# Optimization experiments

Measured on AMD Instinct MI355X. Metric: run time of the kernel, lower is better.

Reference implementation:

```python
import jax, jax.numpy as jnp
import numpy as np

B, TAU, M, NX, NY = 256, 128, 3, 8, 8
N = NX + NY                 # 16 total sensors
D = 2 * N * N               # d_model = 512
NHEAD = 8
DFF = 2048


def _layer_norm(x, g, b, eps=1e-5):
    mu = jnp.mean(x, axis=-1, keepdims=True)
    var = jnp.mean((x - mu) ** 2, axis=-1, keepdims=True)
    return (x - mu) / jnp.sqrt(var + eps) * g + b


def _mha(x, wi, bi, wo, bo):
    Bq, S, Dm = x.shape
    hd = Dm // NHEAD
    qkv = x @ wi.T + bi                         # (B,S,3D)
    q, k, v = jnp.split(qkv, 3, axis=-1)
    sh = lambda t: t.reshape(Bq, S, NHEAD, hd).transpose(0, 2, 1, 3)
    q, k, v = sh(q), sh(k), sh(v)
    att = jax.nn.softmax(jnp.einsum('bhqd,bhkd->bhqk', q, k) / jnp.sqrt(jnp.float32(hd)), axis=-1)
    o = jnp.einsum('bhqk,bhkd->bhqd', att, v).transpose(0, 2, 1, 3).reshape(Bq, S, Dm)
    return o @ wo.T + bo


def poly_roots(c):
    # companion-matrix roots; c[..., 0] is the leading coefficient
    n = c.shape[-1] - 1
    first = (-c[..., 1:] / c[..., :1])[..., None, :]                      # (..., 1, n)
    below = jnp.broadcast_to(jnp.eye(n - 1, n, dtype=c.dtype), c.shape[:-1] + (n - 1, n))
    return jnp.linalg.eigvals(jnp.concatenate([first, below], axis=-2))   # (..., n)


def root_music_doa(Rz, m):
    # Rz: (B, n, n) Hermitian PSD (gram + eps*I) -> eigh == eig sorted by |lambda|
    n = Rz.shape[-1]
    w, v = jnp.linalg.eigh(Rz)                  # ascending real eigenvalues
    Un = v[..., : n - m]                        # noise subspace (smallest n-m)
    F = Un @ jnp.conj(jnp.swapaxes(Un, -1, -2))
    # sum of each diagonal, offsets -(n-1)..(n-1) -> 2n-1 poly coefficients
    coeffs = jnp.stack([jnp.sum(jnp.diagonal(F, offset=o, axis1=-2, axis2=-1), axis=-1)
                        for o in range(-(n - 1), n)], axis=-1)
    roots = poly_roots(coeffs)                  # (B, 2n-2)
    # sort by closeness to unit circle; push roots with |r|>=1 to the back
    keyv = jnp.abs(jnp.abs(roots) - 1.0) + jnp.where(jnp.abs(roots) < 1.0, 0.0, 1e6)
    sel = jnp.take_along_axis(roots, jnp.argsort(keyv, axis=-1)[..., :m], axis=-1)
    # dist=0.5, f=1 -> 1/(2*pi*dist*f) = 1/pi
    return jnp.arcsin(jnp.angle(sel) / jnp.pi)  # (B, m)


def setup_inputs() -> dict:
    key = jax.random.key(0)
    ks = jax.random.split(key, 12)
    rn = lambda k, s: 0.02 * jax.random.normal(k, s, jnp.float32)
    return {
        'Rx_tau': jax.random.normal(ks[0], (B, TAU, 2 * N, N), jnp.float32),
        'in_proj_w': rn(ks[1], (3 * D, D)), 'in_proj_b': jnp.zeros((3 * D,), jnp.float32),
        'out_proj_w': rn(ks[2], (D, D)), 'out_proj_b': jnp.zeros((D,), jnp.float32),
        'ln1_g': jnp.ones((D,), jnp.float32), 'ln1_b': jnp.zeros((D,), jnp.float32),
        'ffn_w1': rn(ks[3], (DFF, D)), 'ffn_b1': jnp.zeros((DFF,), jnp.float32),
        'ffn_w2': rn(ks[4], (D, DFF)), 'ffn_b2': jnp.zeros((D,), jnp.float32),
        'ln2_g': jnp.ones((D,), jnp.float32), 'ln2_b': jnp.zeros((D,), jnp.float32),
        'fcx_w': rn(ks[5], (2 * NX * NX, D)), 'fcx_b': jnp.zeros((2 * NX * NX,), jnp.float32),
        'fcy_w': rn(ks[6], (2 * NY * NY, D)), 'fcy_b': jnp.zeros((2 * NY * NY,), jnp.float32),
        'mlp_w1': rn(ks[7], (256, 2 * M)), 'mlp_b1': jnp.zeros((256,), jnp.float32),
        'mlp_w2': rn(ks[8], (256, 256)), 'mlp_b2': jnp.zeros((256,), jnp.float32),
        'mlp_w3': rn(ks[9], (2 * M, 256)), 'mlp_b3': jnp.zeros((2 * M,), jnp.float32),
    }


def reference(Rx_tau, in_proj_w, in_proj_b, out_proj_w, out_proj_b, ln1_g, ln1_b,
              ffn_w1, ffn_b1, ffn_w2, ffn_b2, ln2_g, ln2_b,
              fcx_w, fcx_b, fcy_w, fcy_b,
              mlp_w1, mlp_b1, mlp_w2, mlp_b2, mlp_w3, mlp_b3):
    x = Rx_tau.reshape(Rx_tau.shape[0], -1, D)  # (B, tau, 512)
    # post-LN TransformerEncoderLayer (eval: dropout off)
    x = _layer_norm(x + _mha(x, in_proj_w, in_proj_b, out_proj_w, out_proj_b), ln1_g, ln1_b)
    ff = jnp.maximum(x @ ffn_w1.T + ffn_b1, 0.0) @ ffn_w2.T + ffn_b2
    x = _layer_norm(x + ff, ln2_g, ln2_b)
    x = jnp.mean(x, axis=1)                     # (B, D)
    Rx = (x @ fcx_w.T + fcx_b).reshape(-1, 2 * NX, NX)
    Ry = (x @ fcy_w.T + fcy_b).reshape(-1, 2 * NY, NY)
    Kx = jax.lax.complex(Rx[:, :NX], Rx[:, NX:])
    Ky = jax.lax.complex(Ry[:, :NY], Ry[:, NY:])
    # gram_diagonal_overload: K^H K + eps*I, eps=1
    Rz_x = jnp.einsum('bji,bjk->bik', jnp.conj(Kx), Kx) + jnp.eye(NX, dtype=Kx.dtype)
    Rz_y = jnp.einsum('bji,bjk->bik', jnp.conj(Ky), Ky) + jnp.eye(NY, dtype=Ky.dtype)
    doa_t = root_music_doa(Rz_x, M)
    doa_p = root_music_doa(Rz_y, M)
    h = jnp.concatenate([doa_t, doa_p], axis=-1).astype(jnp.float32)  # (B, 2M)
    h = jnp.maximum(h @ mlp_w1.T + mlp_b1, 0.0)
    h = jnp.maximum(h @ mlp_w2.T + mlp_b2, 0.0)
    outs = h @ mlp_w3.T + mlp_b3
    return outs[:, :M], outs[:, M:]
```

## Files before the change

kernel.cpp:

```cpp
#include <hip/hip_runtime.h>
#include <math.h>

#define S_LEN 128
#define D_MODEL 512
#define B_SZ 256
#define NHEADS 8
#define HD 64
#define DFFN 2048
#define PI_D 3.14159265358979323846

typedef _Float16 f16x8 __attribute__((ext_vector_type(8)));
typedef _Float16 f16x4 __attribute__((ext_vector_type(4)));
typedef float f32x4 __attribute__((ext_vector_type(4)));

__device__ __forceinline__ void gl_lds(const _Float16* g, _Float16* l) {
    __builtin_amdgcn_global_load_lds(
        (const __attribute__((address_space(1))) void*)g,
        (__attribute__((address_space(3))) void*)l, 16, 0, 0);
}

__global__ __launch_bounds__(256) void cvt_split(const float* __restrict__ in,
        _Float16* __restrict__ hi, _Float16* __restrict__ lo, int n4)
{
    const int i = blockIdx.x * 256 + threadIdx.x;
    if (i >= n4) return;
    float4 v = ((const float4*)in)[i];
    f16x4 h, l;
    _Float16 h0 = (_Float16)v.x; h[0] = h0; l[0] = (_Float16)(v.x - (float)h0);
    _Float16 h1 = (_Float16)v.y; h[1] = h1; l[1] = (_Float16)(v.y - (float)h1);
    _Float16 h2 = (_Float16)v.z; h[2] = h2; l[2] = (_Float16)(v.z - (float)h2);
    _Float16 h3 = (_Float16)v.w; h[3] = h3; l[3] = (_Float16)(v.w - (float)h3);
    ((f16x4*)hi)[i] = h;
    ((f16x4*)lo)[i] = l;
}

template<int OUTMODE>
__global__ __launch_bounds__(256) void gemm_mfma(
        const _Float16* __restrict__ Ahg, const _Float16* __restrict__ Alg,
        const _Float16* __restrict__ Whg, const _Float16* __restrict__ Wlg,
        const float* __restrict__ bias, float* __restrict__ Cf,
        _Float16* __restrict__ Ch, _Float16* __restrict__ Cl,
        int M, int N, int K)
{
    __shared__ _Float16 lds[2][4][8192];
    const int t = threadIdx.x;
    const int lane = t & 63;
    const int w = t >> 6;
    const int wr = w >> 1, wc = w & 1;
    const int row0 = blockIdx.y * 128, col0 = blockIdx.x * 128;

    const int srow = lane >> 3;
    const int schunk = (lane & 7) ^ srow;

    const _Float16* gA[2] = { Ahg, Alg };
    const _Float16* gW[2] = { Whg, Wlg };

    auto stage = [&](int buf, int kt) {
        const int k0 = kt << 6;
#pragma unroll
        for (int a = 0; a < 2; ++a) {
#pragma unroll
            for (int j = 0; j < 4; ++j) {
                const int i = w * 4 + j;
                const int rA = row0 + 8 * i + srow;
                gl_lds(gA[a] + (size_t)rA * K + k0 + schunk * 8,
                       &lds[buf][a][i * 512]);
            }
#pragma unroll
            for (int j = 0; j < 4; ++j) {
                const int i = w * 4 + j;
                const int rW = col0 + 8 * i + srow;
                gl_lds(gW[a] + (size_t)rW * K + k0 + schunk * 8,
                       &lds[buf][2 + a][i * 512]);
            }
        }
    };

    f32x4 acc[4][4];
#pragma unroll
    for (int m = 0; m < 4; ++m)
#pragma unroll
        for (int n = 0; n < 4; ++n) acc[m][n] = (f32x4)0.f;

    const int NT = K >> 6;
    stage(0, 0);
    float bv[4];
#pragma unroll
    for (int n = 0; n < 4; ++n) bv[n] = bias[col0 + wc * 64 + n * 16 + (lane & 15)];

    for (int kt = 0; kt < NT; ++kt) {
        const int cur = kt & 1;
        if (kt + 1 < NT) {
            stage(cur ^ 1, kt + 1);
            asm volatile("s_waitcnt vmcnt(16)" ::: "memory");
        } else {
            asm volatile("s_waitcnt vmcnt(0)" ::: "memory");
        }
        __syncthreads();
#pragma unroll
        for (int ks = 0; ks < 2; ++ks) {
            const int kf = ks * 32 + (lane >> 4) * 8;
            f16x8 afh[4], afl[4], bfh[4], bfl[4];
#pragma unroll
            for (int m = 0; m < 4; ++m) {
                const int row = wr * 64 + m * 16 + (lane & 15);
                const int e = row * 64 + (kf ^ ((row & 7) << 3));
                afh[m] = *(const f16x8*)&lds[cur][0][e];
                afl[m] = *(const f16x8*)&lds[cur][1][e];
            }
#pragma unroll
            for (int n = 0; n < 4; ++n) {
                const int row = wc * 64 + n * 16 + (lane & 15);
                const int e = row * 64 + (kf ^ ((row & 7) << 3));
                bfh[n] = *(const f16x8*)&lds[cur][2][e];
                bfl[n] = *(const f16x8*)&lds[cur][3][e];
            }
#pragma unroll
            for (int m = 0; m < 4; ++m)
#pragma unroll
                for (int n = 0; n < 4; ++n) {
                    acc[m][n] = __builtin_amdgcn_mfma_f32_16x16x32_f16(afh[m], bfh[n], acc[m][n], 0, 0, 0);
                    acc[m][n] = __builtin_amdgcn_mfma_f32_16x16x32_f16(afh[m], bfl[n], acc[m][n], 0, 0, 0);
                    acc[m][n] = __builtin_amdgcn_mfma_f32_16x16x32_f16(afl[m], bfh[n], acc[m][n], 0, 0, 0);
                }
        }
        __syncthreads();
    }

#pragma unroll
    for (int m = 0; m < 4; ++m) {
        const int rowc = row0 + wr * 64 + m * 16 + ((lane >> 4) << 2);
#pragma unroll
        for (int n = 0; n < 4; ++n) {
            const int colc = col0 + wc * 64 + n * 16 + (lane & 15);
#pragma unroll
            for (int j = 0; j < 4; ++j) {
                float v = acc[m][n][j] + bv[n];
                if (OUTMODE == 2) {
                    v = fmaxf(v, 0.f);
                    const size_t idx = (size_t)(rowc + j) * N + colc;
                    _Float16 h = (_Float16)v;
                    Ch[idx] = h;
                    Cl[idx] = (_Float16)(v - (float)h);
                } else {
                    Cf[(size_t)(rowc + j) * N + colc] = v;
                }
            }
        }
    }
}

template<int RELU>
__global__ __launch_bounds__(256) void gemm_bias(const float* __restrict__ A,
        const float* __restrict__ W, const float* __restrict__ bias,
        float* __restrict__ C, int M, int N, int K)
{
    __shared__ float As[8][128];
    __shared__ float Ws[8][128];
    const int tid = threadIdx.x;
    const int tn = tid & 15, tm = tid >> 4;
    const int row0 = blockIdx.y * 128, col0 = blockIdx.x * 128;
    const int lr = tid >> 1, lc = (tid & 1) * 4;
    const float* Ap = A + (size_t)(row0 + lr) * K + lc;
    const float* Wp = W + (size_t)(col0 + lr) * K + lc;
    float acc[8][8];
#pragma unroll
    for (int i = 0; i < 8; ++i)
#pragma unroll
        for (int j = 0; j < 8; ++j) acc[i][j] = 0.f;

    for (int k0 = 0; k0 < K; k0 += 8) {
        float4 av = *(const float4*)(Ap + k0);
        float4 wv = *(const float4*)(Wp + k0);
        __syncthreads();
        As[lc + 0][lr] = av.x; As[lc + 1][lr] = av.y;
        As[lc + 2][lr] = av.z; As[lc + 3][lr] = av.w;
        Ws[lc + 0][lr] = wv.x; Ws[lc + 1][lr] = wv.y;
        Ws[lc + 2][lr] = wv.z; Ws[lc + 3][lr] = wv.w;
        __syncthreads();
#pragma unroll
        for (int k = 0; k < 8; ++k) {
            float ar[8], wrg[8];
#pragma unroll
            for (int i = 0; i < 8; ++i) ar[i] = As[k][tm * 8 + i];
#pragma unroll
            for (int j = 0; j < 8; ++j) wrg[j] = Ws[k][tn * 8 + j];
#pragma unroll
            for (int i = 0; i < 8; ++i)
#pragma unroll
                for (int j = 0; j < 8; ++j)
                    acc[i][j] = fmaf(ar[i], wrg[j], acc[i][j]);
        }
    }
#pragma unroll
    for (int i = 0; i < 8; ++i) {
        const int r = row0 + tm * 8 + i;
#pragma unroll
        for (int j = 0; j < 8; ++j) {
            const int c = col0 + tn * 8 + j;
            float v = acc[i][j] + bias[c];
            if (RELU) v = fmaxf(v, 0.f);
            C[(size_t)r * N + c] = v;
        }
    }
}

__global__ __launch_bounds__(128) void attn_kernel(const float* __restrict__ qkv,
        _Float16* __restrict__ oh, _Float16* __restrict__ ol)
{
    const int bh = blockIdx.x;
    const int b = bh >> 3, hh = bh & 7;
    const int t = threadIdx.x;
    __shared__ float Ks[S_LEN][HD];
    __shared__ float Vs[S_LEN][HD];
    const float* base = qkv + (size_t)b * S_LEN * (3 * D_MODEL);
    const float* krow = base + (size_t)t * (3 * D_MODEL) + D_MODEL + hh * HD;
    const float* vrow = base + (size_t)t * (3 * D_MODEL) + 2 * D_MODEL + hh * HD;
#pragma unroll
    for (int d = 0; d < HD; d += 4) {
        *(float4*)&Ks[t][d] = *(const float4*)(krow + d);
        *(float4*)&Vs[t][d] = *(const float4*)(vrow + d);
    }
    float q[HD];
    const float* qrow = base + (size_t)t * (3 * D_MODEL) + hh * HD;
#pragma unroll
    for (int d = 0; d < HD; d += 4) {
        float4 v4 = *(const float4*)(qrow + d);
        q[d] = v4.x; q[d + 1] = v4.y; q[d + 2] = v4.z; q[d + 3] = v4.w;
    }
    __syncthreads();
    float m = -1e30f, l = 0.f;
    float oacc[HD];
#pragma unroll
    for (int d = 0; d < HD; ++d) oacc[d] = 0.f;
    for (int j = 0; j < S_LEN; ++j) {
        float s = 0.f;
#pragma unroll
        for (int d = 0; d < HD; ++d) s = fmaf(q[d], Ks[j][d], s);
        s *= 0.125f;
        const float nm = fmaxf(m, s);
        const float sc = expf(m - nm);
        const float p = expf(s - nm);
        l = l * sc + p;
#pragma unroll
        for (int d = 0; d < HD; ++d) oacc[d] = oacc[d] * sc + p * Vs[j][d];
        m = nm;
    }
    const float inv = 1.f / l;
    const size_t ob = (size_t)b * S_LEN * D_MODEL + (size_t)t * D_MODEL + hh * HD;
#pragma unroll
    for (int d = 0; d < HD; ++d) {
        const float v = oacc[d] * inv;
        const _Float16 h = (_Float16)v;
        oh[ob + d] = h;
        ol[ob + d] = (_Float16)(v - (float)h);
    }
}

template<int SPLIT>
__global__ __launch_bounds__(128) void add_ln_kernel(const float* __restrict__ a,
        const float* __restrict__ bb, const float* __restrict__ g,
        const float* __restrict__ be, float* __restrict__ out,
        _Float16* __restrict__ oh, _Float16* __restrict__ ol)
{
    __shared__ float red[2];
    const int row = blockIdx.x, t = threadIdx.x;
    float4 av = *(const float4*)(a + (size_t)row * D_MODEL + t * 4);
    float4 bv = *(const float4*)(bb + (size_t)row * D_MODEL + t * 4);
    float x0 = av.x + bv.x, x1 = av.y + bv.y, x2 = av.z + bv.z, x3 = av.w + bv.w;
    float ssum = x0 + x1 + x2 + x3;
#pragma unroll
    for (int off = 32; off >= 1; off >>= 1) ssum += __shfl_xor(ssum, off);
    if ((t & 63) == 0) red[t >> 6] = ssum;
    __syncthreads();
    const float mean = (red[0] + red[1]) * (1.f / 512.f);
    __syncthreads();
    float d0 = x0 - mean, d1 = x1 - mean, d2 = x2 - mean, d3 = x3 - mean;
    float sq = d0 * d0 + d1 * d1 + d2 * d2 + d3 * d3;
#pragma unroll
    for (int off = 32; off >= 1; off >>= 1) sq += __shfl_xor(sq, off);
    if ((t & 63) == 0) red[t >> 6] = sq;
    __syncthreads();
    const float var = (red[0] + red[1]) * (1.f / 512.f);
    const float inv = 1.0f / sqrtf(var + 1e-5f);
    float4 gv = *(const float4*)(g + t * 4);
    float4 bev = *(const float4*)(be + t * 4);
    float4 ov = make_float4(d0 * inv * gv.x + bev.x, d1 * inv * gv.y + bev.y,
                            d2 * inv * gv.z + bev.z, d3 * inv * gv.w + bev.w);
    *(float4*)(out + (size_t)row * D_MODEL + t * 4) = ov;
    if (SPLIT) {
        f16x4 h, l;
        _Float16 h0 = (_Float16)ov.x; h[0] = h0; l[0] = (_Float16)(ov.x - (float)h0);
        _Float16 h1 = (_Float16)ov.y; h[1] = h1; l[1] = (_Float16)(ov.y - (float)h1);
        _Float16 h2 = (_Float16)ov.z; h[2] = h2; l[2] = (_Float16)(ov.z - (float)h2);
        _Float16 h3 = (_Float16)ov.w; h[3] = h3; l[3] = (_Float16)(ov.w - (float)h3);
        *(f16x4*)&oh[(size_t)row * D_MODEL + t * 4] = h;
        *(f16x4*)&ol[(size_t)row * D_MODEL + t * 4] = l;
    }
}

__global__ __launch_bounds__(128) void pool_kernel(const float* __restrict__ x,
                                                   float* __restrict__ pooled)
{
    const int b = blockIdx.x, t = threadIdx.x;
    float4 acc = make_float4(0.f, 0.f, 0.f, 0.f);
    const float* base = x + (size_t)b * S_LEN * D_MODEL + t * 4;
    for (int s = 0; s < S_LEN; ++s) {
        float4 v = *(const float4*)(base + (size_t)s * D_MODEL);
        acc.x += v.x; acc.y += v.y; acc.z += v.z; acc.w += v.w;
    }
    const float sc = 1.f / 128.f;
    float4 ov = make_float4(acc.x * sc, acc.y * sc, acc.z * sc, acc.w * sc);
    *(float4*)(pooled + (size_t)b * D_MODEL + t * 4) = ov;
}

__global__ __launch_bounds__(64) void music_kernel(const float* __restrict__ RxRy,
                                                   float* __restrict__ hbuf)
{
    const int pb = blockIdx.x;
    const int b = pb >> 1, which = pb & 1;
    const float* src = RxRy + (size_t)which * (B_SZ * 128) + (size_t)b * 128;
    const int t = threadIdx.x;
    const int i = t >> 3, j = t & 7;

    __shared__ double KRe[8][8], KIm[8][8];
    __shared__ double Ar[8][8], Ai[8][8], Vr[8][8], Vi[8][8];
    __shared__ double Fre[8][8], Fim[8][8];
    __shared__ double rc[4], rs[4], rer[4], rei[4];
    __shared__ double cr[15], ci[15], br[14], bi[14], zr[14], zi[14];
    __shared__ int topidx[3];

    KRe[i][j] = (double)src[i * 8 + j];
    KIm[i][j] = (double)src[64 + i * 8 + j];
    __syncthreads();
    {
        double sre = (i == j) ? 1.0 : 0.0, sim = 0.0;
        for (int r = 0; r < 8; ++r) {
            const double ar = KRe[r][i], ai = KIm[r][i];
            const double xr = KRe[r][j], xi = KIm[r][j];
            sre += ar * xr + ai * xi;
            sim += ar * xi - ai * xr;
        }
        Ar[i][j] = sre; Ai[i][j] = sim;
        Vr[i][j] = (i == j) ? 1.0 : 0.0;
        Vi[i][j] = 0.0;
    }
    __syncthreads();

    for (int sw = 0; sw < 9; ++sw)
    for (int rr = 0; rr < 7; ++rr) {
        int pp[4], qq[4];
        pp[0] = 0;                 qq[0] = (rr + 6) % 7 + 1;
        pp[1] = rr % 7 + 1;        qq[1] = (rr + 5) % 7 + 1;
        pp[2] = (rr + 1) % 7 + 1;  qq[2] = (rr + 4) % 7 + 1;
        pp[3] = (rr + 2) % 7 + 1;  qq[3] = (rr + 3) % 7 + 1;
        if (t < 4) {
            const int p = pp[t], q = qq[t];
            const double gre = Ar[p][q], gim = Ai[p][q];
            const double r = sqrt(gre * gre + gim * gim);
            double c, s, er, ei;
            if (r < 1e-60) { c = 1.0; s = 0.0; er = 1.0; ei = 0.0; }
            else {
                const double tau = (Ar[p][p] - Ar[q][q]) / (2.0 * r);
                const double tt = ((tau >= 0.0) ? 1.0 : -1.0) /
                                  (fabs(tau) + sqrt(1.0 + tau * tau));
                c = 1.0 / sqrt(1.0 + tt * tt); s = tt * c;
                er = gre / r; ei = gim / r;
            }
            rc[t] = c; rs[t] = s; rer[t] = er; rei[t] = ei;
        }
        __syncthreads();
        int gi = 0, gj = 0;
#pragma unroll
        for (int g = 0; g < 4; ++g) {
            if (pp[g] == i || qq[g] == i) gi = g;
            if (pp[g] == j || qq[g] == j) gj = g;
        }
        const int ri_q = (qq[gi] == i), rj_q = (qq[gj] == j);
        const double ci_ = rc[gi], si_ = rs[gi], eir = rer[gi], eii = rei[gi];
        const double cj_ = rc[gj], sj_ = rs[gj], ejr = rer[gj], eji = rei[gj];
        const int Pi = pp[gi], Qi = qq[gi], Pj = pp[gj], Qj = qq[gj];

        double bPr, bPi_, bQr, bQi_;
        {
            double apr = Ar[Pi][Pj], api = Ai[Pi][Pj];
            double aqr = Ar[Pi][Qj], aqi = Ai[Pi][Qj];
            if (!rj_q) { bPr = cj_ * apr + sj_ * (ejr * aqr + eji * aqi);
                         bPi_= cj_ * api + sj_ * (ejr * aqi - eji * aqr); }
            else       { bPr = cj_ * aqr - sj_ * (ejr * apr - eji * api);
                         bPi_= cj_ * aqi - sj_ * (ejr * api + eji * apr); }
            apr = Ar[Qi][Pj]; api = Ai[Qi][Pj];
            aqr = Ar[Qi][Qj]; aqi = Ai[Qi][Qj];
            if (!rj_q) { bQr = cj_ * apr + sj_ * (ejr * aqr + eji * aqi);
                         bQi_= cj_ * api + sj_ * (ejr * aqi - eji * aqr); }
            else       { bQr = cj_ * aqr - sj_ * (ejr * apr - eji * api);
                         bQi_= cj_ * aqi - sj_ * (ejr * api + eji * apr); }
        }
        double nAr, nAi_;
        if (!ri_q) { nAr = ci_ * bPr + si_ * (eir * bQr - eii * bQi_);
                     nAi_= ci_ * bPi_+ si_ * (eir * bQi_ + eii * bQr); }
        else       { nAr = ci_ * bQr - si_ * (eir * bPr + eii * bPi_);
                     nAi_= ci_ * bQi_- si_ * (eir * bPi_ - eii * bPr); }
        double nVr, nVi_;
        {
            const double vpr = Vr[i][Pj], vpi = Vi[i][Pj];
            const double vqr = Vr[i][Qj], vqi = Vi[i][Qj];
            if (!rj_q) { nVr = cj_ * vpr + sj_ * (ejr * vqr + eji * vqi);
                         nVi_= cj_ * vpi + sj_ * (ejr * vqi - eji * vqr); }
            else       { nVr = cj_ * vqr - sj_ * (ejr * vpr - eji * vpi);
                         nVi_= cj_ * vqi - sj_ * (ejr * vpi + eji * vpr); }
        }
        __syncthreads();
        Ar[i][j] = nAr; Ai[i][j] = nAi_;
        Vr[i][j] = nVr; Vi[i][j] = nVi_;
        __syncthreads();
    }

    if (t == 0) {
        bool used[8] = {false, false, false, false, false, false, false, false};
        for (int tt = 0; tt < 3; ++tt) {
            double best = -1e300; int bidx = 0;
            for (int k = 0; k < 8; ++k)
                if (!used[k] && Ar[k][k] > best) { best = Ar[k][k]; bidx = k; }
            used[bidx] = true; topidx[tt] = bidx;
        }
    }
    __syncthreads();
    {
        double fre = (i == j) ? 1.0 : 0.0, fim = 0.0;
        for (int tt = 0; tt < 3; ++tt) {
            const int e = topidx[tt];
            const double vir = Vr[i][e], vii = Vi[i][e];
            const double vjr = Vr[j][e], vji = Vi[j][e];
            fre -= vir * vjr + vii * vji;
            fim -= vii * vjr - vir * vji;
        }
        Fre[i][j] = fre; Fim[i][j] = fim;
    }
    __syncthreads();
    if (t < 15) {
        const int o = t - 7;
        double sre = 0.0, sim = 0.0;
        for (int r = 0; r < 8; ++r) {
            const int cc = r + o;
            if (cc >= 0 && cc < 8) { sre += Fre[r][cc]; sim += Fim[r][cc]; }
        }
        cr[t] = sre; ci[t] = sim;
    }
    __syncthreads();
    if (t < 14) {
        const double den = cr[0] * cr[0] + ci[0] * ci[0];
        const double nr = cr[t + 1], ni = ci[t + 1];
        br[t] = (nr * cr[0] + ni * ci[0]) / den;
        bi[t] = (ni * cr[0] - nr * ci[0]) / den;
        double zre_ = 1.0, zim_ = 0.0;
        for (int k = 0; k <= t; ++k) {
            const double a2 = zre_ * 0.4 - zim_ * 0.9;
            zim_ = zre_ * 0.9 + zim_ * 0.4;
            zre_ = a2;
        }
        zr[t] = zre_; zi[t] = zim_;
    }
    __syncthreads();
    for (int it = 0; it < 128; ++it) {
        double nzr = 0.0, nzi = 0.0;
        if (t < 14) {
            const double zre_ = zr[t], zim_ = zi[t];
            double wre = 1.0, wim = 0.0;
            for (int k = 0; k < 14; ++k) {
                const double tr = wre * zre_ - wim * zim_ + br[k];
                wim = wre * zim_ + wim * zre_ + bi[k];
                wre = tr;
            }
            double dre = 1.0, dim = 0.0;
            for (int k = 0; k < 14; ++k) {
                if (k == t) continue;
                const double exr = zre_ - zr[k], exi = zim_ - zi[k];
                const double tr = dre * exr - dim * exi;
                dim = dre * exi + dim * exr;
                dre = tr;
            }
            const double dd = dre * dre + dim * dim;
            if (dd > 1e-260) {
                const double qre = (wre * dre + wim * dim) / dd;
                const double qim = (wim * dre - wre * dim) / dd;
                nzr = zre_ - qre; nzi = zim_ - qim;
            } else {
                nzr = zre_ + 1e-8; nzi = zim_ - 1e-8;
            }
        }
        __syncthreads();
        if (t < 14) { zr[t] = nzr; zi[t] = nzi; }
        __syncthreads();
    }
    if (t == 0) {
        double keyv[14]; bool used[14];
        for (int k = 0; k < 14; ++k) {
            const double mag = sqrt(zr[k] * zr[k] + zi[k] * zi[k]);
            keyv[k] = fabs(mag - 1.0) + ((mag < 1.0) ? 0.0 : 1e6);
            used[k] = false;
        }
        for (int tt = 0; tt < 3; ++tt) {
            double best = 1e300; int bidx = 0;
            for (int k = 0; k < 14; ++k)
                if (!used[k] && keyv[k] < best) { best = keyv[k]; bidx = k; }
            used[bidx] = true;
            const double ang = atan2(zi[bidx], zr[bidx]);
            double ratio = ang / PI_D;
            if (ratio > 1.0) ratio = 1.0;
            if (ratio < -1.0) ratio = -1.0;
            hbuf[(size_t)b * 6 + which * 3 + tt] = (float)asin(ratio);
        }
    }
}

__global__ __launch_bounds__(256) void mlp_kernel(const float* __restrict__ hbuf,
        const float* __restrict__ w1, const float* __restrict__ b1,
        const float* __restrict__ w2, const float* __restrict__ b2,
        const float* __restrict__ w3, const float* __restrict__ b3,
        float* __restrict__ outp)
{
    const int b = blockIdx.x, t = threadIdx.x;
    __shared__ float hin[8];
    __shared__ float h1[256];
    __shared__ float h2[256];
    if (t < 6) hin[t] = hbuf[b * 6 + t];
    __syncthreads();
    float acc = b1[t];
#pragma unroll
    for (int k = 0; k < 6; ++k) acc += hin[k] * w1[t * 6 + k];
    h1[t] = fmaxf(acc, 0.f);
    __syncthreads();
    float acc2 = b2[t];
    for (int k = 0; k < 256; ++k) acc2 += h1[k] * w2[t * 256 + k];
    h2[t] = fmaxf(acc2, 0.f);
    __syncthreads();
    if (t < 6) {
        float acc3 = b3[t];
        for (int k = 0; k < 256; ++k) acc3 += h2[k] * w3[t * 256 + k];
        if (t < 3) outp[b * 3 + t] = acc3;
        else       outp[B_SZ * 3 + b * 3 + (t - 3)] = acc3;
    }
}

extern "C" void kernel_launch(void* const* d_in, const int* in_sizes, int n_in,
                              void* d_out, int out_size, void* d_ws, size_t ws_size,
                              hipStream_t stream)
{
    const float* x_in      = (const float*)d_in[0];
    const float* in_proj_w = (const float*)d_in[1];
    const float* in_proj_b = (const float*)d_in[2];
    const float* out_proj_w= (const float*)d_in[3];
    const float* out_proj_b= (const float*)d_in[4];
    const float* ln1_g     = (const float*)d_in[5];
    const float* ln1_b     = (const float*)d_in[6];
    const float* ffn_w1    = (const float*)d_in[7];
    const float* ffn_b1    = (const float*)d_in[8];
    const float* ffn_w2    = (const float*)d_in[9];
    const float* ffn_b2    = (const float*)d_in[10];
    const float* ln2_g     = (const float*)d_in[11];
    const float* ln2_b     = (const float*)d_in[12];
    const float* fcx_w     = (const float*)d_in[13];
    const float* fcx_b     = (const float*)d_in[14];
    const float* fcy_w     = (const float*)d_in[15];
    const float* fcy_b     = (const float*)d_in[16];
    const float* mlp_w1    = (const float*)d_in[17];
    const float* mlp_b1    = (const float*)d_in[18];
    const float* mlp_w2    = (const float*)d_in[19];
    const float* mlp_b2    = (const float*)d_in[20];
    const float* mlp_w3    = (const float*)d_in[21];
    const float* mlp_b3    = (const float*)d_in[22];

    const size_t N_IPW = 1536 * 512, N_OPW = 512 * 512;
    const size_t N_F1W = 2048 * 512, N_F2W = 512 * 2048;
    const size_t WCVT = N_IPW + N_OPW + N_F1W + N_F2W;
    float* ws = (float*)d_ws;
    _Float16* ipw_h = (_Float16*)ws;
    _Float16* ipw_l = ipw_h + N_IPW;
    _Float16* opw_h = ipw_l + N_IPW;
    _Float16* opw_l = opw_h + N_OPW;
    _Float16* f1w_h = opw_l + N_OPW;
    _Float16* f1w_l = f1w_h + N_F1W;
    _Float16* f2w_h = f1w_l + N_F1W;
    _Float16* f2w_l = f2w_h + N_F2W;
    float* dyn = ws + WCVT;

    const size_t ws_floats = ws_size / sizeof(float);
    int c = 256;
    while (c > 1 && (size_t)524288 * (size_t)c + 262144 + WCVT > ws_floats) c >>= 1;

    float* R0     = dyn;
    float* xhf    = R0 + (size_t)262144 * c;
    float* xlf    = xhf + (size_t)32768 * c;
    float* x1     = xlf + (size_t)32768 * c;
    float* x1hf   = x1 + (size_t)65536 * c;
    float* x1lf   = x1hf + (size_t)32768 * c;
    float* ff2    = x1lf + (size_t)32768 * c;
    float* pooled = ff2 + (size_t)65536 * c;
    float* RxRy   = pooled + 131072;
    float* hbuf   = RxRy + 65536;

    float*    qkv  = R0;
    _Float16* oh   = (_Float16*)(R0 + (size_t)196608 * c);
    _Float16* ol   = oh + (size_t)65536 * c;
    _Float16* ff1h = (_Float16*)R0;
    _Float16* ff1l = ff1h + (size_t)262144 * c;
    _Float16* xh   = (_Float16*)xhf;
    _Float16* xl   = (_Float16*)xlf;
    _Float16* x1h  = (_Float16*)x1hf;
    _Float16* x1l  = (_Float16*)x1lf;

    cvt_split<<<(N_IPW / 4 + 255) / 256, 256, 0, stream>>>(in_proj_w,  ipw_h, ipw_l, N_IPW / 4);
    cvt_split<<<(N_OPW / 4 + 255) / 256, 256, 0, stream>>>(out_proj_w, opw_h, opw_l, N_OPW / 4);
    cvt_split<<<(N_F1W / 4 + 255) / 256, 256, 0, stream>>>(ffn_w1,     f1w_h, f1w_l, N_F1W / 4);
    cvt_split<<<(N_F2W / 4 + 255) / 256, 256, 0, stream>>>(ffn_w2,     f2w_h, f2w_l, N_F2W / 4);

    for (int b0 = 0; b0 < B_SZ; b0 += c) {
        const int Tc = c * S_LEN;
        const float* xc = x_in + (size_t)b0 * S_LEN * D_MODEL;
        const int n4x = Tc * D_MODEL / 4;

        cvt_split<<<(n4x + 255) / 256, 256, 0, stream>>>(xc, xh, xl, n4x);
        gemm_mfma<0><<<dim3(1536 / 128, Tc / 128), 256, 0, stream>>>(
            xh, xl, ipw_h, ipw_l, in_proj_b, qkv, nullptr, nullptr, Tc, 3 * D_MODEL, D_MODEL);
        attn_kernel<<<c * NHEADS, 128, 0, stream>>>(qkv, oh, ol);
        gemm_mfma<0><<<dim3(512 / 128, Tc / 128), 256, 0, stream>>>(
            oh, ol, opw_h, opw_l, out_proj_b, x1, nullptr, nullptr, Tc, D_MODEL, D_MODEL);
        add_ln_kernel<1><<<Tc, 128, 0, stream>>>(xc, x1, ln1_g, ln1_b, x1, x1h, x1l);
        gemm_mfma<2><<<dim3(DFFN / 128, Tc / 128), 256, 0, stream>>>(
            x1h, x1l, f1w_h, f1w_l, ffn_b1, nullptr, ff1h, ff1l, Tc, DFFN, D_MODEL);
        gemm_mfma<0><<<dim3(512 / 128, Tc / 128), 256, 0, stream>>>(
            ff1h, ff1l, f2w_h, f2w_l, ffn_b2, ff2, nullptr, nullptr, Tc, D_MODEL, DFFN);
        add_ln_kernel<0><<<Tc, 128, 0, stream>>>(x1, ff2, ln2_g, ln2_b, x1, nullptr, nullptr);
        pool_kernel<<<c, 128, 0, stream>>>(x1, pooled + (size_t)b0 * D_MODEL);
    }

    gemm_bias<0><<<dim3(1, 2), 256, 0, stream>>>(
        pooled, fcx_w, fcx_b, RxRy, B_SZ, 128, D_MODEL);
    gemm_bias<0><<<dim3(1, 2), 256, 0, stream>>>(
        pooled, fcy_w, fcy_b, RxRy + B_SZ * 128, B_SZ, 128, D_MODEL);
    music_kernel<<<2 * B_SZ, 64, 0, stream>>>(RxRy, hbuf);
    mlp_kernel<<<B_SZ, 256, 0, stream>>>(hbuf, mlp_w1, mlp_b1, mlp_w2, mlp_b2,
                                         mlp_w3, mlp_b3, (float*)d_out);
}
```

Measured before the change: 1.821 ms.

## Shrink MFMA GEMM K-tile to 32 and split Durand-Kerner across four lanes

The split-fp16 MFMA GEMM now stages 32-wide K tiles instead of 64. Each wave loads one of the four operand planes with an unswizzled layout, which halves LDS use and doubles the number of pipeline iterations. The Durand-Kerner root iteration now uses 4 lanes per root instead of one. The polynomial is evaluated as interleaved Horner in z^4 and the product of root differences is split across lanes, with both combined via shuffles, to shorten the serial fp64 dependency chain. Dropping the XOR swizzle may add LDS bank conflicts, and the shorter K tiles add more barriers per GEMM.

```diff
diff --git a/kernel.cpp b/kernel.cpp
--- a/kernel.cpp
+++ b/kernel.cpp
@@ -42,38 +42,25 @@
         _Float16* __restrict__ Ch, _Float16* __restrict__ Cl,
         int M, int N, int K)
 {
-    __shared__ _Float16 lds[2][4][8192];
+    __shared__ _Float16 lds[2][4][4096];
     const int t = threadIdx.x;
     const int lane = t & 63;
     const int w = t >> 6;
     const int wr = w >> 1, wc = w & 1;
     const int row0 = blockIdx.y * 128, col0 = blockIdx.x * 128;
 
-    const int srow = lane >> 3;
-    const int schunk = (lane & 7) ^ srow;
-
-    const _Float16* gA[2] = { Ahg, Alg };
-    const _Float16* gW[2] = { Whg, Wlg };
+    const _Float16* gptr[4] = { Ahg, Alg, Whg, Wlg };
+    const int rbase = (w < 2) ? row0 : col0;
+    const _Float16* gsrc = gptr[w];
+    const int lr = lane >> 2;
+    const int lc = (lane & 3) * 8;
 
     auto stage = [&](int buf, int kt) {
-        const int k0 = kt << 6;
-#pragma unroll
-        for (int a = 0; a < 2; ++a) {
-#pragma unroll
-            for (int j = 0; j < 4; ++j) {
-                const int i = w * 4 + j;
-                const int rA = row0 + 8 * i + srow;
-                gl_lds(gA[a] + (size_t)rA * K + k0 + schunk * 8,
-                       &lds[buf][a][i * 512]);
-            }
-#pragma unroll
-            for (int j = 0; j < 4; ++j) {
-                const int i = w * 4 + j;
-                const int rW = col0 + 8 * i + srow;
-                gl_lds(gW[a] + (size_t)rW * K + k0 + schunk * 8,
-                       &lds[buf][2 + a][i * 512]);
-            }
-        }
+        const _Float16* srcb = gsrc + (size_t)(rbase + lr) * K + (kt << 5) + lc;
+        _Float16* dstb = &lds[buf][w][lane * 8];
+#pragma unroll
+        for (int p = 0; p < 8; ++p)
+            gl_lds(srcb + (size_t)p * 16 * K, dstb + p * 512);
     };
 
     f32x4 acc[4][4];
@@ -82,48 +69,43 @@
 #pragma unroll
         for (int n = 0; n < 4; ++n) acc[m][n] = (f32x4)0.f;
 
-    const int NT = K >> 6;
+    const int NT = K >> 5;
     stage(0, 0);
     float bv[4];
 #pragma unroll
     for (int n = 0; n < 4; ++n) bv[n] = bias[col0 + wc * 64 + n * 16 + (lane & 15)];
 
+    const int kf = (lane >> 4) * 8;
     for (int kt = 0; kt < NT; ++kt) {
         const int cur = kt & 1;
         if (kt + 1 < NT) {
             stage(cur ^ 1, kt + 1);
-            asm volatile("s_waitcnt vmcnt(16)" ::: "memory");
+            asm volatile("s_waitcnt vmcnt(8)" ::: "memory");
         } else {
             asm volatile("s_waitcnt vmcnt(0)" ::: "memory");
         }
         __syncthreads();
-#pragma unroll
-        for (int ks = 0; ks < 2; ++ks) {
-            const int kf = ks * 32 + (lane >> 4) * 8;
-            f16x8 afh[4], afl[4], bfh[4], bfl[4];
-#pragma unroll
-            for (int m = 0; m < 4; ++m) {
-                const int row = wr * 64 + m * 16 + (lane & 15);
-                const int e = row * 64 + (kf ^ ((row & 7) << 3));
-                afh[m] = *(const f16x8*)&lds[cur][0][e];
-                afl[m] = *(const f16x8*)&lds[cur][1][e];
+        f16x8 afh[4], afl[4], bfh[4], bfl[4];
+#pragma unroll
+        for (int m = 0; m < 4; ++m) {
+            const int e = (wr * 64 + m * 16 + (lane & 15)) * 32 + kf;
+            afh[m] = *(const f16x8*)&lds[cur][0][e];
+            afl[m] = *(const f16x8*)&lds[cur][1][e];
+        }
+#pragma unroll
+        for (int n = 0; n < 4; ++n) {
+            const int e = (wc * 64 + n * 16 + (lane & 15)) * 32 + kf;
+            bfh[n] = *(const f16x8*)&lds[cur][2][e];
+            bfl[n] = *(const f16x8*)&lds[cur][3][e];
+        }
+#pragma unroll
+        for (int m = 0; m < 4; ++m)
+#pragma unroll
+            for (int n = 0; n < 4; ++n) {
+                acc[m][n] = __builtin_amdgcn_mfma_f32_16x16x32_f16(afh[m], bfh[n], acc[m][n], 0, 0, 0);
+                acc[m][n] = __builtin_amdgcn_mfma_f32_16x16x32_f16(afh[m], bfl[n], acc[m][n], 0, 0, 0);
+                acc[m][n] = __builtin_amdgcn_mfma_f32_16x16x32_f16(afl[m], bfh[n], acc[m][n], 0, 0, 0);
             }
-#pragma unroll
-            for (int n = 0; n < 4; ++n) {
-                const int row = wc * 64 + n * 16 + (lane & 15);
-                const int e = row * 64 + (kf ^ ((row & 7) << 3));
-                bfh[n] = *(const f16x8*)&lds[cur][2][e];
-                bfl[n] = *(const f16x8*)&lds[cur][3][e];
-            }
-#pragma unroll
-            for (int m = 0; m < 4; ++m)
-#pragma unroll
-                for (int n = 0; n < 4; ++n) {
-                    acc[m][n] = __builtin_amdgcn_mfma_f32_16x16x32_f16(afh[m], bfh[n], acc[m][n], 0, 0, 0);
-                    acc[m][n] = __builtin_amdgcn_mfma_f32_16x16x32_f16(afh[m], bfl[n], acc[m][n], 0, 0, 0);
-                    acc[m][n] = __builtin_amdgcn_mfma_f32_16x16x32_f16(afl[m], bfh[n], acc[m][n], 0, 0, 0);
-                }
-        }
         __syncthreads();
     }
 
@@ -160,9 +142,9 @@
     const int tid = threadIdx.x;
     const int tn = tid & 15, tm = tid >> 4;
     const int row0 = blockIdx.y * 128, col0 = blockIdx.x * 128;
-    const int lr = tid >> 1, lc = (tid & 1) * 4;
-    const float* Ap = A + (size_t)(row0 + lr) * K + lc;
-    const float* Wp = W + (size_t)(col0 + lr) * K + lc;
+    const int lrr = tid >> 1, lcc = (tid & 1) * 4;
+    const float* Ap = A + (size_t)(row0 + lrr) * K + lcc;
+    const float* Wp = W + (size_t)(col0 + lrr) * K + lcc;
     float acc[8][8];
 #pragma unroll
     for (int i = 0; i < 8; ++i)
@@ -173,10 +155,10 @@
         float4 av = *(const float4*)(Ap + k0);
         float4 wv = *(const float4*)(Wp + k0);
         __syncthreads();
-        As[lc + 0][lr] = av.x; As[lc + 1][lr] = av.y;
-        As[lc + 2][lr] = av.z; As[lc + 3][lr] = av.w;
-        Ws[lc + 0][lr] = wv.x; Ws[lc + 1][lr] = wv.y;
-        Ws[lc + 2][lr] = wv.z; Ws[lc + 3][lr] = wv.w;
+        As[lcc + 0][lrr] = av.x; As[lcc + 1][lrr] = av.y;
+        As[lcc + 2][lrr] = av.z; As[lcc + 3][lrr] = av.w;
+        Ws[lcc + 0][lrr] = wv.x; Ws[lcc + 1][lrr] = wv.y;
+        Ws[lcc + 2][lrr] = wv.z; Ws[lcc + 3][lrr] = wv.w;
         __syncthreads();
 #pragma unroll
         for (int k = 0; k < 8; ++k) {
@@ -462,37 +444,66 @@
         zr[t] = zre_; zi[t] = zim_;
     }
     __syncthreads();
+
+    const int rt = t >> 2, jj = t & 3;
+    const int rsafe = (rt < 14) ? rt : 0;
+    double A_r[4], A_i[4];
+#pragma unroll
+    for (int m = 0; m < 4; ++m) {
+        const int idx = 13 - 4 * m - jj;
+        if (idx >= 0)       { A_r[m] = br[idx]; A_i[m] = bi[idx]; }
+        else if (idx == -1) { A_r[m] = 1.0;     A_i[m] = 0.0; }
+        else                { A_r[m] = 0.0;     A_i[m] = 0.0; }
+    }
+    const int k0 = jj * 4, k1 = (jj == 3) ? 14 : jj * 4 + 4;
+
     for (int it = 0; it < 128; ++it) {
-        double nzr = 0.0, nzi = 0.0;
-        if (t < 14) {
-            const double zre_ = zr[t], zim_ = zi[t];
-            double wre = 1.0, wim = 0.0;
-            for (int k = 0; k < 14; ++k) {
-                const double tr = wre * zre_ - wim * zim_ + br[k];
-                wim = wre * zim_ + wim * zre_ + bi[k];
-                wre = tr;
-            }
-            double dre = 1.0, dim = 0.0;
-            for (int k = 0; k < 14; ++k) {
-                if (k == t) continue;
-                const double exr = zre_ - zr[k], exi = zim_ - zi[k];
-                const double tr = dre * exr - dim * exi;
-                dim = dre * exi + dim * exr;
-                dre = tr;
-            }
-            const double dd = dre * dre + dim * dim;
-            if (dd > 1e-260) {
-                const double qre = (wre * dre + wim * dim) / dd;
-                const double qim = (wim * dre - wre * dim) / dd;
-                nzr = zre_ - qre; nzi = zim_ - qim;
-            } else {
-                nzr = zre_ + 1e-8; nzi = zim_ - 1e-8;
-            }
-        }
-        __syncthreads();
-        if (t < 14) { zr[t] = nzr; zi[t] = nzi; }
-        __syncthreads();
-    }
+        const double zre = zr[rsafe], zim = zi[rsafe];
+        const double z2r = zre * zre - zim * zim, z2i = 2.0 * zre * zim;
+        const double yr = z2r * z2r - z2i * z2i, yi = 2.0 * z2r * z2i;
+        double wre = A_r[3], wim = A_i[3];
+#pragma unroll
+        for (int m = 2; m >= 0; --m) {
+            const double tr = wre * yr - wim * yi + A_r[m];
+            wim = wre * yi + wim * yr + A_i[m];
+            wre = tr;
+        }
+        double pr, pi;
+        if (jj == 0)      { pr = wre; pi = wim; }
+        else if (jj == 1) { pr = wre * zre - wim * zim; pi = wre * zim + wim * zre; }
+        else if (jj == 2) { pr = wre * z2r - wim * z2i; pi = wre * z2i + wim * z2r; }
+        else { const double z3r = z2r * zre - z2i * zim, z3i = z2r * zim + z2i * zre;
+               pr = wre * z3r - wim * z3i; pi = wre * z3i + wim * z3r; }
+        pr += __shfl_xor(pr, 1); pi += __shfl_xor(pi, 1);
+        pr += __shfl_xor(pr, 2); pi += __shfl_xor(pi, 2);
+        double dr = 1.0, di = 0.0;
+        for (int k = k0; k < k1; ++k) {
+            if (k == rsafe) continue;
+            const double exr = zre - zr[k], exi = zim - zi[k];
+            const double tr = dr * exr - di * exi;
+            di = dr * exi + di * exr;
+            dr = tr;
+        }
+        {
+            double orr = __shfl_xor(dr, 1), oii = __shfl_xor(di, 1);
+            double tr = dr * orr - di * oii; di = dr * oii + di * orr; dr = tr;
+            orr = __shfl_xor(dr, 2); oii = __shfl_xor(di, 2);
+            tr = dr * orr - di * oii; di = dr * oii + di * orr; dr = tr;
+        }
+        double nzr, nzi;
+        const double dd = dr * dr + di * di;
+        if (dd > 1e-260) {
+            const double qre = (pr * dr + pi * di) / dd;
+            const double qim = (pi * dr - pr * di) / dd;
+            nzr = zre - qre; nzi = zim - qim;
+        } else {
+            nzr = zre + 1e-8; nzi = zim - 1e-8;
+        }
+        __syncthreads();
+        if (t < 56 && jj == 0) { zr[rt] = nzr; zi[rt] = nzi; }
+        __syncthreads();
+    }
+
     if (t == 0) {
         double keyv[14]; bool used[14];
         for (int k = 0; k < 14; ++k) {
```

New measurement: 1.786 ms. Within noise of the previous version (-1.9%).
